# Kernel tuning notes

Hardware: AMD Instinct MI355X
Metric: run time of the kernel (lower is better)

Reference implementation:

```python
import jax, jax.numpy as jnp
import numpy as np

IN_DIM = 1024
OUT_DIM = 1024
NUM_COEFFS = 32 + 3  # grid_size + spline_order


def setup_inputs() -> dict:
    key = jax.random.key(0)
    k1, k2, k3 = jax.random.split(key, 3)
    x = jax.random.normal(k1, (4096, IN_DIM), dtype=jnp.float32)
    spline_weight = jax.random.normal(k2, (IN_DIM, OUT_DIM, NUM_COEFFS), dtype=jnp.float32) * 0.1
    base_scale = jax.random.normal(k3, (IN_DIM, OUT_DIM), dtype=jnp.float32) * 0.1
    grid = jnp.linspace(-1.0, 1.0, NUM_COEFFS, dtype=jnp.float32)
    return {"x": x, "spline_weight": spline_weight, "base_scale": base_scale, "grid": grid}


def _b_spline_cubic(x, grid):
    # x: [b, i] -> basis [b, i, c]
    h = 2.0 / (NUM_COEFFS - 1)
    dist = jnp.abs(x[..., None] - grid) / h
    inner = 2.0 / 3.0 - dist * dist + dist * dist * dist * 0.5
    t = 2.0 - dist
    outer = t * t * t / 6.0
    return jnp.where(dist < 1.0, inner, jnp.where(dist < 2.0, outer, 0.0))


def reference(x, spline_weight, base_scale, grid):
    x_norm = jnp.clip(x, -0.99, 0.99)
    base_act = jax.nn.silu(x_norm)                      # [b, i]
    base_out = jnp.einsum('bi,ij->bj', base_act, base_scale)
    basis = _b_spline_cubic(x_norm, grid)               # [b, i, c]
    spline_out = jnp.einsum('bic,ijc->bj', basis, spline_weight)
    return base_out + spline_out
```

## Files before the change

### kernel.cpp

```cpp
#include <hip/hip_runtime.h>
#include <hip/hip_bf16.h>


#define IN_DIM 1024
#define OUT_DIM 1024
#define NC 35
#define KPI 36
#define KTOT (IN_DIM * KPI)
#define MROWS 4096
#define BM 128
#define BN 128
#define BK 32
#define NSPLIT 4
#define KCH (KTOT / NSPLIT)
#define NSTEP (KCH / BK)

#define BKPA 40

typedef __attribute__((ext_vector_type(8))) __bf16 bf16x8;
typedef __attribute__((ext_vector_type(4))) float f32x4;

__device__ __forceinline__ unsigned short f2bf(float f) {
  unsigned int u = __builtin_bit_cast(unsigned int, f);
  u = (u + 0x7FFFu + ((u >> 16) & 1u)) >> 16;
  return (unsigned short)u;
}

__global__ __launch_bounds__(256) void prep_wb(const float* __restrict__ sw,
                                               const float* __restrict__ bs,
                                               unsigned short* __restrict__ wb) {
  int id = blockIdx.x * 256 + threadIdx.x;
  int i = id & (IN_DIM - 1);
  int n = id >> 10;
  const float* s = sw + (size_t)i * (OUT_DIM * NC) + (size_t)n * NC;
  unsigned short v[KPI];
#pragma unroll
  for (int c = 0; c < NC; ++c) v[c] = f2bf(s[c]);
  v[NC] = f2bf(bs[(size_t)i * OUT_DIM + n]);
  uint2* dst = (uint2*)(wb + (size_t)n * KTOT + (size_t)i * KPI);
#pragma unroll
  for (int w = 0; w < 9; ++w) {
    uint2 t;
    t.x = (unsigned)v[4 * w + 0] | ((unsigned)v[4 * w + 1] << 16);
    t.y = (unsigned)v[4 * w + 2] | ((unsigned)v[4 * w + 3] << 16);
    dst[w] = t;
  }
}

__global__ __launch_bounds__(256) void prep_a(const float* __restrict__ x,
                                              unsigned short* __restrict__ A) {
  __shared__ unsigned short buf[256 * KPI];
  const int tid = threadIdx.x;
  const int id = blockIdx.x * 256 + tid;
  float xv = x[id];
  float xn = fminf(fmaxf(xv, -0.99f), 0.99f);
  float u = (xn + 1.0f) * 17.0f;
  float sf = floorf(u);
  int s = (int)sf;
  float f = u - sf, g = 1.0f - f;
  float f2 = f * f, g2 = g * g;
  float v0 = g2 * g * (1.f / 6.f);
  float v1 = 0.66666667f - f2 + 0.5f * f2 * f;
  float v2 = 0.66666667f - g2 + 0.5f * g2 * g;
  float v3 = f2 * f * (1.f / 6.f);
  float sig = xn / (1.0f + __expf(-xn));

  unsigned short* row = buf + tid * KPI;
  uint2 z = make_uint2(0, 0);
  uint2* rz = (uint2*)row;
#pragma unroll
  for (int w = 0; w < 9; ++w) rz[w] = z;
#pragma unroll
  for (int t = 0; t < 4; ++t) {
    int c = s - 1 + t;
    float v = (t == 0) ? v0 : (t == 1) ? v1 : (t == 2) ? v2 : v3;
    if (c >= 0 && c < NC) row[c] = f2bf(v);
  }
  row[NC] = f2bf(sig);
  __syncthreads();
  uint2* gdst = (uint2*)(A + (size_t)blockIdx.x * (256 * KPI));
  const uint2* gsrc = (const uint2*)buf;
#pragma unroll
  for (int w = 0; w < 9; ++w) gdst[tid + w * 256] = gsrc[tid + w * 256];
}

__global__ __launch_bounds__(256) void kan_gemm_pre(const unsigned short* __restrict__ A,
                                                    const unsigned short* __restrict__ wb,
                                                    float* __restrict__ out) {
  __shared__ __align__(16) unsigned short As[BM * BK];
  __shared__ __align__(16) unsigned short Ws[BN * BK];

  const int tid = threadIdx.x;
  const int mt = blockIdx.x, nt = blockIdx.y, kc = blockIdx.z;

  const int lane = tid & 63;
  const int wid = tid >> 6;
  const int wm = (wid & 1) * 64;
  const int wn = (wid >> 1) * 64;
  const int lm = lane & 15;
  const int quad = lane >> 4;
  const int ko = quad * 8;

  const int wr16 = lane >> 2;
  const int wkof = (lane & 3) * 8;

  f32x4 acc[4][4];
#pragma unroll
  for (int a = 0; a < 4; ++a)
#pragma unroll
    for (int b = 0; b < 4; ++b) acc[a][b] = f32x4{0.f, 0.f, 0.f, 0.f};

  const unsigned short* Abase =
      A + (size_t)(mt * BM + wid * 32 + wr16) * KTOT + kc * KCH + wkof;
  const unsigned short* Wbase =
      wb + (size_t)(nt * BN + wid * 32 + wr16) * KTOT + kc * KCH + wkof;

  for (int step = 0; step < NSTEP; ++step) {
    const int kof = step * BK;
#pragma unroll
    for (int c = 0; c < 2; ++c) {
      __builtin_amdgcn_global_load_lds(
          (const __attribute__((address_space(1))) unsigned int*)(Abase + (size_t)c * 16 * KTOT + kof),
          (__attribute__((address_space(3))) unsigned int*)(&As[(wid * 32 + c * 16) * BK]),
          16, 0, 0);
    }
#pragma unroll
    for (int c = 0; c < 2; ++c) {
      __builtin_amdgcn_global_load_lds(
          (const __attribute__((address_space(1))) unsigned int*)(Wbase + (size_t)c * 16 * KTOT + kof),
          (__attribute__((address_space(3))) unsigned int*)(&Ws[(wid * 32 + c * 16) * BK]),
          16, 0, 0);
    }
    __syncthreads();

    uint4 af[4], bfr[4];
#pragma unroll
    for (int mi = 0; mi < 4; ++mi)
      af[mi] = *(const uint4*)(&As[(wm + mi * 16 + lm) * BK + ko]);
#pragma unroll
    for (int ni = 0; ni < 4; ++ni)
      bfr[ni] = *(const uint4*)(&Ws[(wn + ni * 16 + lm) * BK + ko]);
#pragma unroll
    for (int mi = 0; mi < 4; ++mi)
#pragma unroll
      for (int ni = 0; ni < 4; ++ni)
        acc[mi][ni] = __builtin_amdgcn_mfma_f32_16x16x32_bf16(
            __builtin_bit_cast(bf16x8, af[mi]), __builtin_bit_cast(bf16x8, bfr[ni]),
            acc[mi][ni], 0, 0, 0);

    __syncthreads();
  }

#pragma unroll
  for (int mi = 0; mi < 4; ++mi)
#pragma unroll
    for (int ni = 0; ni < 4; ++ni)
#pragma unroll
      for (int r = 0; r < 4; ++r) {
        int row = mt * BM + wm + mi * 16 + quad * 4 + r;
        int col = nt * BN + wn + ni * 16 + lm;
        atomicAdd(&out[(size_t)row * OUT_DIM + col], acc[mi][ni][r]);
      }
}

template <bool USE_WB>
__global__ __launch_bounds__(256) void kan_gemm(const float* __restrict__ x,
                                                const unsigned short* __restrict__ wb,
                                                const float* __restrict__ sw,
                                                const float* __restrict__ bs,
                                                float* __restrict__ out) {
  __shared__ __align__(16) unsigned short As[BM * BKPA];
  __shared__ __align__(16) unsigned short Ws[BN * BKPA];

  const int tid = threadIdx.x;
  const int mt = blockIdx.x, nt = blockIdx.y, kc = blockIdx.z;
  const int sb = tid & 127;
  const int shalf = tid >> 7;
  const int klo = shalf * 16;
  const int wrow = tid >> 1;
  const int whal = tid & 1;
  const int lane = tid & 63;
  const int wid = tid >> 6;
  const int wm = (wid & 1) * 64;
  const int wn = (wid >> 1) * 64;
  const int lm = lane & 15;
  const int quad = lane >> 4;
  const int ko = quad * 8;

  f32x4 acc[4][4];
#pragma unroll
  for (int a = 0; a < 4; ++a)
#pragma unroll
    for (int b = 0; b < 4; ++b) acc[a][b] = f32x4{0.f, 0.f, 0.f, 0.f};

  const float* xrow = x + (size_t)(mt * BM + sb) * IN_DIM;

  for (int step = 0; step < NSTEP; ++step) {
    const int kbase = kc * KCH + step * BK;
    {
      uint4 z = make_uint4(0, 0, 0, 0);
      uint4* az = (uint4*)(&As[sb * BKPA + klo]);
      az[0] = z;
      az[1] = z;
    }
    {
      const int ilo = kbase / KPI;
      const int ihi = (kbase + BK - 1) / KPI;
      for (int ii = ilo; ii <= ihi; ++ii) {
        float xv = xrow[ii];
        float xn = fminf(fmaxf(xv, -0.99f), 0.99f);
        float u = (xn + 1.0f) * 17.0f;
        float sf = floorf(u);
        int s = (int)sf;
        float f = u - sf, g = 1.0f - f;
        float f2 = f * f, g2 = g * g;
        float v0 = g2 * g * (1.f / 6.f);
        float v1 = 0.66666667f - f2 + 0.5f * f2 * f;
        float v2 = 0.66666667f - g2 + 0.5f * g2 * g;
        float v3 = f2 * f * (1.f / 6.f);
        float sig = xn / (1.0f + __expf(-xn));
        const int kb0 = ii * KPI - kbase;
#pragma unroll
        for (int t = 0; t < 4; ++t) {
          int c = s - 1 + t;
          float v = (t == 0) ? v0 : (t == 1) ? v1 : (t == 2) ? v2 : v3;
          int kq = kb0 + c;
          if (c >= 0 && c < NC && kq >= klo && kq < klo + 16)
            As[sb * BKPA + kq] = f2bf(v);
        }
        int kqb = kb0 + NC;
        if (kqb >= klo && kqb < klo + 16) As[sb * BKPA + kqb] = f2bf(sig);
      }
    }
    if (USE_WB) {
      const unsigned short* src = wb + (size_t)(nt * BN + wrow) * KTOT + kbase + whal * 16;
      uint4 w0 = ((const uint4*)src)[0];
      uint4 w1 = ((const uint4*)src)[1];
      uint4* wd = (uint4*)(&Ws[wrow * BKPA + whal * 16]);
      wd[0] = w0;
      wd[1] = w1;
    } else {
      const int j = nt * BN + wrow;
      unsigned int p[8];
#pragma unroll
      for (int q = 0; q < 8; ++q) {
        unsigned int lohi = 0;
#pragma unroll
        for (int h = 0; h < 2; ++h) {
          int k = kbase + whal * 16 + q * 2 + h;
          int i = k / KPI;
          int c = k - i * KPI;
          float v = (c < NC) ? sw[(size_t)i * (OUT_DIM * NC) + (size_t)j * NC + c]
                             : bs[(size_t)i * OUT_DIM + j];
          lohi |= ((unsigned int)f2bf(v)) << (16 * h);
        }
        p[q] = lohi;
      }
      uint4* wd = (uint4*)(&Ws[wrow * BKPA + whal * 16]);
      wd[0] = make_uint4(p[0], p[1], p[2], p[3]);
      wd[1] = make_uint4(p[4], p[5], p[6], p[7]);
    }

    __syncthreads();

    uint4 af[4], bfr[4];
#pragma unroll
    for (int mi = 0; mi < 4; ++mi)
      af[mi] = *(const uint4*)(&As[(wm + mi * 16 + lm) * BKPA + ko]);
#pragma unroll
    for (int ni = 0; ni < 4; ++ni)
      bfr[ni] = *(const uint4*)(&Ws[(wn + ni * 16 + lm) * BKPA + ko]);
#pragma unroll
    for (int mi = 0; mi < 4; ++mi)
#pragma unroll
      for (int ni = 0; ni < 4; ++ni)
        acc[mi][ni] = __builtin_amdgcn_mfma_f32_16x16x32_bf16(
            __builtin_bit_cast(bf16x8, af[mi]), __builtin_bit_cast(bf16x8, bfr[ni]),
            acc[mi][ni], 0, 0, 0);

    __syncthreads();
  }

#pragma unroll
  for (int mi = 0; mi < 4; ++mi)
#pragma unroll
    for (int ni = 0; ni < 4; ++ni)
#pragma unroll
      for (int r = 0; r < 4; ++r) {
        int row = mt * BM + wm + mi * 16 + quad * 4 + r;
        int col = nt * BN + wn + ni * 16 + lm;
        atomicAdd(&out[(size_t)row * OUT_DIM + col], acc[mi][ni][r]);
      }
}

extern "C" void kernel_launch(void* const* d_in, const int* in_sizes, int n_in,
                              void* d_out, int out_size, void* d_ws, size_t ws_size,
                              hipStream_t stream) {
  const float* x = (const float*)d_in[0];
  const float* sw = (const float*)d_in[1];
  const float* bs = (const float*)d_in[2];
  float* out = (float*)d_out;

  hipMemsetAsync(d_out, 0, (size_t)MROWS * OUT_DIM * sizeof(float), stream);

  const size_t WB_BYTES = (size_t)OUT_DIM * KTOT * sizeof(unsigned short);
  const size_t A_BYTES = (size_t)MROWS * KTOT * sizeof(unsigned short);
  dim3 grid(MROWS / BM, OUT_DIM / BN, NSPLIT);

  if (ws_size >= WB_BYTES + A_BYTES) {
    unsigned short* wbp = (unsigned short*)d_ws;
    unsigned short* ap = (unsigned short*)((char*)d_ws + WB_BYTES);
    prep_wb<<<(IN_DIM * OUT_DIM) / 256, 256, 0, stream>>>(sw, bs, wbp);
    prep_a<<<(MROWS * IN_DIM) / 256, 256, 0, stream>>>(x, ap);
    kan_gemm_pre<<<grid, 256, 0, stream>>>(ap, wbp, out);
  } else if (ws_size >= WB_BYTES) {
    unsigned short* wbp = (unsigned short*)d_ws;
    prep_wb<<<(IN_DIM * OUT_DIM) / 256, 256, 0, stream>>>(sw, bs, wbp);
    kan_gemm<true><<<grid, 256, 0, stream>>>(x, wbp, sw, bs, out);
  } else {
    kan_gemm<false><<<grid, 256, 0, stream>>>(x, nullptr, sw, bs, out);
  }
}
```

Baseline: 854.7 us.

## Triple-buffer GEMM LDS loads and coalesce weight-prep reads through shared memory

The precomputed-operand GEMM now keeps three LDS stages. It issues the next tile's global-to-LDS loads before computing on the current one and uses a partial vmcnt wait plus a barrier in place of two syncthreads per step. prep_wb is remapped so each block loads a contiguous slab of spline weights into shared memory with coalesced reads, then packs each output row from LDS. This targets memory latency stalls in the main loop and uncoalesced strided reads in weight prep, at the cost of more LDS per block and hand-written waitcnt synchronisation.

Result: faster. 833.1 us (-2.5%).

```diff
diff --git a/kernel.cpp b/kernel.cpp
--- a/kernel.cpp
+++ b/kernel.cpp
@@ -29,21 +29,26 @@
 __global__ __launch_bounds__(256) void prep_wb(const float* __restrict__ sw,
                                                const float* __restrict__ bs,
                                                unsigned short* __restrict__ wb) {
-  int id = blockIdx.x * 256 + threadIdx.x;
-  int i = id & (IN_DIM - 1);
-  int n = id >> 10;
-  const float* s = sw + (size_t)i * (OUT_DIM * NC) + (size_t)n * NC;
+  __shared__ float sb[256 * NC];
+  const int tid = threadIdx.x;
+  const int i = blockIdx.x;
+  const int n0 = blockIdx.y * 256;
+  const float* src = sw + ((size_t)i * OUT_DIM + n0) * NC;
+  for (int t = tid; t < 256 * NC; t += 256) sb[t] = src[t];
+  float bv = bs[(size_t)i * OUT_DIM + n0 + tid];
+  __syncthreads();
   unsigned short v[KPI];
-#pragma unroll
-  for (int c = 0; c < NC; ++c) v[c] = f2bf(s[c]);
-  v[NC] = f2bf(bs[(size_t)i * OUT_DIM + n]);
-  uint2* dst = (uint2*)(wb + (size_t)n * KTOT + (size_t)i * KPI);
+  const float* mine = sb + tid * NC;
+#pragma unroll
+  for (int c = 0; c < NC; ++c) v[c] = f2bf(mine[c]);
+  v[NC] = f2bf(bv);
+  uint2* dst = (uint2*)(wb + (size_t)(n0 + tid) * KTOT + i * KPI);
 #pragma unroll
   for (int w = 0; w < 9; ++w) {
-    uint2 t;
-    t.x = (unsigned)v[4 * w + 0] | ((unsigned)v[4 * w + 1] << 16);
-    t.y = (unsigned)v[4 * w + 2] | ((unsigned)v[4 * w + 3] << 16);
-    dst[w] = t;
+    uint2 t2;
+    t2.x = (unsigned)v[4 * w + 0] | ((unsigned)v[4 * w + 1] << 16);
+    t2.y = (unsigned)v[4 * w + 2] | ((unsigned)v[4 * w + 3] << 16);
+    dst[w] = t2;
   }
 }
 
@@ -84,11 +89,11 @@
   for (int w = 0; w < 9; ++w) gdst[tid + w * 256] = gsrc[tid + w * 256];
 }
 
-__global__ __launch_bounds__(256) void kan_gemm_pre(const unsigned short* __restrict__ A,
-                                                    const unsigned short* __restrict__ wb,
-                                                    float* __restrict__ out) {
-  __shared__ __align__(16) unsigned short As[BM * BK];
-  __shared__ __align__(16) unsigned short Ws[BN * BK];
+__global__ __launch_bounds__(256) void kan_gemm_db(const unsigned short* __restrict__ A,
+                                                   const unsigned short* __restrict__ wb,
+                                                   float* __restrict__ out) {
+  __shared__ __align__(16) unsigned short As[3][BM * BK];
+  __shared__ __align__(16) unsigned short Ws[3][BN * BK];
 
   const int tid = threadIdx.x;
   const int mt = blockIdx.x, nt = blockIdx.y, kc = blockIdx.z;
@@ -110,36 +115,43 @@
 #pragma unroll
     for (int b = 0; b < 4; ++b) acc[a][b] = f32x4{0.f, 0.f, 0.f, 0.f};
 
-  const unsigned short* Abase =
+  const unsigned short* Ab =
       A + (size_t)(mt * BM + wid * 32 + wr16) * KTOT + kc * KCH + wkof;
-  const unsigned short* Wbase =
+  const unsigned short* Wg =
       wb + (size_t)(nt * BN + wid * 32 + wr16) * KTOT + kc * KCH + wkof;
 
+  auto issue = [&](int buf, int koff) {
+#pragma unroll
+    for (int c = 0; c < 2; ++c)
+      __builtin_amdgcn_global_load_lds(
+          (const __attribute__((address_space(1))) unsigned int*)(Ab + (size_t)c * 16 * KTOT + koff),
+          (__attribute__((address_space(3))) unsigned int*)(&As[buf][(wid * 32 + c * 16) * BK]),
+          16, 0, 0);
+#pragma unroll
+    for (int c = 0; c < 2; ++c)
+      __builtin_amdgcn_global_load_lds(
+          (const __attribute__((address_space(1))) unsigned int*)(Wg + (size_t)c * 16 * KTOT + koff),
+          (__attribute__((address_space(3))) unsigned int*)(&Ws[buf][(wid * 32 + c * 16) * BK]),
+          16, 0, 0);
+  };
+
+  issue(0, 0);
+  int cur = 0, nxt = 1;
   for (int step = 0; step < NSTEP; ++step) {
-    const int kof = step * BK;
-#pragma unroll
-    for (int c = 0; c < 2; ++c) {
-      __builtin_amdgcn_global_load_lds(
-          (const __attribute__((address_space(1))) unsigned int*)(Abase + (size_t)c * 16 * KTOT + kof),
-          (__attribute__((address_space(3))) unsigned int*)(&As[(wid * 32 + c * 16) * BK]),
-          16, 0, 0);
+    if (step + 1 < NSTEP) {
+      issue(nxt, (step + 1) * BK);
+      asm volatile("s_waitcnt vmcnt(4) lgkmcnt(0)\ns_barrier" ::: "memory");
+    } else {
+      asm volatile("s_waitcnt vmcnt(0) lgkmcnt(0)\ns_barrier" ::: "memory");
     }
-#pragma unroll
-    for (int c = 0; c < 2; ++c) {
-      __builtin_amdgcn_global_load_lds(
-          (const __attribute__((address_space(1))) unsigned int*)(Wbase + (size_t)c * 16 * KTOT + kof),
-          (__attribute__((address_space(3))) unsigned int*)(&Ws[(wid * 32 + c * 16) * BK]),
-          16, 0, 0);
-    }
-    __syncthreads();
 
     uint4 af[4], bfr[4];
 #pragma unroll
     for (int mi = 0; mi < 4; ++mi)
-      af[mi] = *(const uint4*)(&As[(wm + mi * 16 + lm) * BK + ko]);
+      af[mi] = *(const uint4*)(&As[cur][(wm + mi * 16 + lm) * BK + ko]);
 #pragma unroll
     for (int ni = 0; ni < 4; ++ni)
-      bfr[ni] = *(const uint4*)(&Ws[(wn + ni * 16 + lm) * BK + ko]);
+      bfr[ni] = *(const uint4*)(&Ws[cur][(wn + ni * 16 + lm) * BK + ko]);
 #pragma unroll
     for (int mi = 0; mi < 4; ++mi)
 #pragma unroll
@@ -148,7 +160,8 @@
             __builtin_bit_cast(bf16x8, af[mi]), __builtin_bit_cast(bf16x8, bfr[ni]),
             acc[mi][ni], 0, 0, 0);
 
-    __syncthreads();
+    cur = nxt;
+    nxt = (nxt == 2) ? 0 : nxt + 1;
   }
 
 #pragma unroll
@@ -170,7 +183,7 @@
                                                 const float* __restrict__ bs,
                                                 float* __restrict__ out) {
   __shared__ __align__(16) unsigned short As[BM * BKPA];
-  __shared__ __align__(16) unsigned short Ws[BN * BKPA];
+  __shared__ __align__(16) unsigned short Wsm[BN * BKPA];
 
   const int tid = threadIdx.x;
   const int mt = blockIdx.x, nt = blockIdx.y, kc = blockIdx.z;
@@ -236,7 +249,7 @@
       const unsigned short* src = wb + (size_t)(nt * BN + wrow) * KTOT + kbase + whal * 16;
       uint4 w0 = ((const uint4*)src)[0];
       uint4 w1 = ((const uint4*)src)[1];
-      uint4* wd = (uint4*)(&Ws[wrow * BKPA + whal * 16]);
+      uint4* wd = (uint4*)(&Wsm[wrow * BKPA + whal * 16]);
       wd[0] = w0;
       wd[1] = w1;
     } else {
@@ -256,7 +269,7 @@
         }
         p[q] = lohi;
       }
-      uint4* wd = (uint4*)(&Ws[wrow * BKPA + whal * 16]);
+      uint4* wd = (uint4*)(&Wsm[wrow * BKPA + whal * 16]);
       wd[0] = make_uint4(p[0], p[1], p[2], p[3]);
       wd[1] = make_uint4(p[4], p[5], p[6], p[7]);
     }
@@ -269,7 +282,7 @@
       af[mi] = *(const uint4*)(&As[(wm + mi * 16 + lm) * BKPA + ko]);
 #pragma unroll
     for (int ni = 0; ni < 4; ++ni)
-      bfr[ni] = *(const uint4*)(&Ws[(wn + ni * 16 + lm) * BKPA + ko]);
+      bfr[ni] = *(const uint4*)(&Wsm[(wn + ni * 16 + lm) * BKPA + ko]);
 #pragma unroll
     for (int mi = 0; mi < 4; ++mi)
 #pragma unroll
@@ -310,12 +323,12 @@
   if (ws_size >= WB_BYTES + A_BYTES) {
     unsigned short* wbp = (unsigned short*)d_ws;
     unsigned short* ap = (unsigned short*)((char*)d_ws + WB_BYTES);
-    prep_wb<<<(IN_DIM * OUT_DIM) / 256, 256, 0, stream>>>(sw, bs, wbp);
+    prep_wb<<<dim3(IN_DIM, OUT_DIM / 256), 256, 0, stream>>>(sw, bs, wbp);
     prep_a<<<(MROWS * IN_DIM) / 256, 256, 0, stream>>>(x, ap);
-    kan_gemm_pre<<<grid, 256, 0, stream>>>(ap, wbp, out);
+    kan_gemm_db<<<grid, 256, 0, stream>>>(ap, wbp, out);
   } else if (ws_size >= WB_BYTES) {
     unsigned short* wbp = (unsigned short*)d_ws;
-    prep_wb<<<(IN_DIM * OUT_DIM) / 256, 256, 0, stream>>>(sw, bs, wbp);
+    prep_wb<<<dim3(IN_DIM, OUT_DIM / 256), 256, 0, stream>>>(sw, bs, wbp);
     kan_gemm<true><<<grid, 256, 0, stream>>>(x, wbp, sw, bs, out);
   } else {
     kan_gemm<false><<<grid, 256, 0, stream>>>(x, nullptr, sw, bs, out);
```
